# Optimization experiments

Hardware: AMD Instinct MI355X
Metric: run time of the kernel (lower is better)

Reference implementation:

```python
import jax, jax.numpy as jnp
import numpy as np

H = 1024     # hidden_size
NH = 16      # num heads
HD = H // NH # head_dim = 64
I = 4096     # intermediate_size
EPS = 1e-6


def rmsnorm(x, w, eps=EPS):
    var = jnp.mean(jnp.square(x), axis=-1, keepdims=True)
    return x * jax.lax.rsqrt(var + eps) * w


def attention(x, ctx, wq, wk, wv, wo):
    # x: [B,S,H], ctx: [B,Skv,H]; weights stored [in,out]
    B, S, _ = x.shape
    Skv = ctx.shape[1]
    q = (x @ wq).reshape(B, S, NH, HD)
    k = (ctx @ wk).reshape(B, Skv, NH, HD)
    v = (ctx @ wv).reshape(B, Skv, NH, HD)
    scores = jnp.einsum('bqhd,bkhd->bhqk', q, k) * (HD ** -0.5)
    attn = jax.nn.softmax(scores.astype(jnp.float32), axis=-1).astype(q.dtype)
    out = jnp.einsum('bhqk,bkhd->bqhd', attn, v).reshape(B, S, NH * HD)
    return out @ wo


def mlp(x, wg, wu, wd):
    return (jax.nn.silu(x @ wg) * (x @ wu)) @ wd


def setup_inputs() -> dict:
    key = jax.random.key(0)
    ks = jax.random.split(key, 16)
    p = lambda k, shape: (jax.random.normal(k, shape, jnp.float32) * 0.02)
    return {
        'hidden_states': jax.random.normal(ks[0], (1, 2048, H), jnp.float32),
        'context': jax.random.normal(ks[1], (1, 2048, H), jnp.float32),
        'sa_norm_w': jnp.ones((H,), jnp.float32),
        'sa_wq': p(ks[2], (H, NH * HD)),
        'sa_wk': p(ks[3], (H, NH * HD)),
        'sa_wv': p(ks[4], (H, NH * HD)),
        'sa_wo': p(ks[5], (NH * HD, H)),
        'ca_norm_w': jnp.ones((H,), jnp.float32),
        'ca_wq': p(ks[6], (H, NH * HD)),
        'ca_wk': p(ks[7], (H, NH * HD)),
        'ca_wv': p(ks[8], (H, NH * HD)),
        'ca_wo': p(ks[9], (NH * HD, H)),
        'mlp_norm_w': jnp.ones((H,), jnp.float32),
        'w_gate': p(ks[10], (H, I)),
        'w_up': p(ks[11], (H, I)),
        'w_down': p(ks[12], (I, H)),
    }


def reference(hidden_states, context, sa_norm_w, sa_wq, sa_wk, sa_wv, sa_wo,
              ca_norm_w, ca_wq, ca_wk, ca_wv, ca_wo,
              mlp_norm_w, w_gate, w_up, w_down):
    # self-attention block
    residual = hidden_states
    h = rmsnorm(hidden_states, sa_norm_w)
    h = residual + attention(h, h, sa_wq, sa_wk, sa_wv, sa_wo)
    # cross-attention block
    residual = h
    hn = rmsnorm(h, ca_norm_w)
    h = residual + attention(hn, context, ca_wq, ca_wk, ca_wv, ca_wo)
    # MLP block
    residual = h
    hn = rmsnorm(h, mlp_norm_w)
    h = residual + mlp(hn, w_gate, w_up, w_down)
    return h
```

## Files before the change

kernel.cpp:

```cpp
#include <hip/hip_runtime.h>

#define H 1024
#define S 2048
#define NH 16
#define HD 64
#define ISZ 4096

typedef __attribute__((ext_vector_type(8))) short s8v;
typedef __attribute__((ext_vector_type(4))) short s4v;
typedef __attribute__((ext_vector_type(4))) float f4v;

__device__ __forceinline__ short f2bf(float f) {
    unsigned u = __builtin_bit_cast(unsigned, f);
    unsigned r = (u + 0x7FFFu + ((u >> 16) & 1u)) >> 16;
    return (short)r;
}
__device__ __forceinline__ float bf2f(short s) {
    unsigned u = ((unsigned)(unsigned short)s) << 16;
    return __builtin_bit_cast(float, u);
}

__device__ __forceinline__ void gload_lds16(const short* g, short* l) {
    __builtin_amdgcn_global_load_lds(
        (const __attribute__((address_space(1))) void*)g,
        (__attribute__((address_space(3))) void*)l, 16, 0, 0);
}

struct PreArgs {
    const void* hid; const void* ctx;
    const void* sanw; const void* canw; const void* mlpnw;
    const void* w[11];
    short* hidc; short* ctxc; short* xn;
    short* canw_o; short* mlpnw_o;
    short* wT[11];
    int* flag_out;
};

__device__ __forceinline__ void tr_tile(const void* src, short* dst, int K, int N,
                                        int k0, int n0, int rmul, int roff,
                                        int isbf, float* tile ) {
    int t = threadIdx.x;
    int c = t & 31, r0 = t >> 5;
    if (isbf) {
        const short* s = (const short*)src;
#pragma unroll
        for (int i = 0; i < 4; i++)
            tile[(r0 + i * 8) * 33 + c] = bf2f(s[(k0 + r0 + i * 8) * N + n0 + c]);
    } else {
        const float* s = (const float*)src;
#pragma unroll
        for (int i = 0; i < 4; i++)
            tile[(r0 + i * 8) * 33 + c] = s[(k0 + r0 + i * 8) * N + n0 + c];
    }
    __syncthreads();
#pragma unroll
    for (int i = 0; i < 4; i++)
        dst[((n0 + r0 + i * 8) * rmul + roff) * K + k0 + c] = f2bf(tile[c * 33 + r0 + i * 8]);
}

__global__ __launch_bounds__(256) void preamble_kernel(PreArgs pa) {
    __shared__ float tile[32 * 33];
    __shared__ float red[4];
    int b = blockIdx.x;
    int t = threadIdx.x;
    int isbf = (((const unsigned*)pa.sanw)[0] == 0x3F803F80u);
    if (blockIdx.x == 0 && t == 0) pa.flag_out[0] = isbf;

    if (b < 2048) {
        int row = b;
        float xf[4];
        if (isbf) {
            s4v xv = *(const s4v*)((const short*)pa.hid + row * H + t * 4);
#pragma unroll
            for (int j = 0; j < 4; j++) xf[j] = bf2f(xv[j]);
        } else {
            const float* s = (const float*)pa.hid + row * H + t * 4;
#pragma unroll
            for (int j = 0; j < 4; j++) xf[j] = s[j];
        }
        float ss = 0.f;
        s4v cv;
#pragma unroll
        for (int j = 0; j < 4; j++) { cv[j] = f2bf(xf[j]); xf[j] = bf2f(cv[j]); ss += xf[j] * xf[j]; }
        *(s4v*)(pa.hidc + row * H + t * 4) = cv;
        int lane = t & 63, wid = t >> 6;
#pragma unroll
        for (int off = 32; off >= 1; off >>= 1) ss += __shfl_xor(ss, off);
        if (lane == 0) red[wid] = ss;
        __syncthreads();
        float tot = red[0] + red[1] + red[2] + red[3];
        float scale = rsqrtf(tot * (1.f / (float)H) + 1e-6f);
        float wv[4];
        if (isbf) {
            s4v wq = *(const s4v*)((const short*)pa.sanw + t * 4);
#pragma unroll
            for (int j = 0; j < 4; j++) wv[j] = bf2f(wq[j]);
        } else {
            const float* s = (const float*)pa.sanw + t * 4;
#pragma unroll
            for (int j = 0; j < 4; j++) wv[j] = s[j];
        }
        s4v ov;
#pragma unroll
        for (int j = 0; j < 4; j++) ov[j] = f2bf(xf[j] * scale * wv[j]);
        *(s4v*)(pa.xn + row * H + t * 4) = ov;
        return;
    }
    b -= 2048;
    if (b < 1024) {
        int i8 = b * 2048 + t * 8;
        if (isbf) {
            *(s8v*)(pa.ctxc + i8) = *(const s8v*)((const short*)pa.ctx + i8);
        } else {
            const float* s = (const float*)pa.ctx;
            s8v o;
#pragma unroll
            for (int j = 0; j < 8; j++) o[j] = f2bf(s[i8 + j]);
            *(s8v*)(pa.ctxc + i8) = o;
        }
        return;
    }
    b -= 1024;
    if (b < 2) {
        const void* src = (b == 0) ? pa.canw : pa.mlpnw;
        short* dst = (b == 0) ? pa.canw_o : pa.mlpnw_o;
        if (isbf) { if (t * 4 < H) *(s4v*)(dst + t * 4) = *(const s4v*)((const short*)src + t * 4); }
        else {
            const float* s = (const float*)src;
            s4v o;
#pragma unroll
            for (int j = 0; j < 4; j++) o[j] = f2bf(s[t * 4 + j]);
            *(s4v*)(dst + t * 4) = o;
        }
        return;
    }
    b -= 2;
    if (b < 8 * 1024) {
        int w = b >> 10, tl = b & 1023;
        tr_tile(pa.w[w], pa.wT[w], H, H, (tl & 31) * 32, (tl >> 5) * 32, 1, 0, isbf, tile);
        return;
    }
    b -= 8 * 1024;
    if (b < 2 * 4096) {
        int w = 8 + (b >> 12), tl = b & 4095;
        tr_tile(pa.w[w], pa.wT[8], H, ISZ, (tl & 31) * 32, (tl >> 5) * 32, 2, w - 8, isbf, tile);
        return;
    }
    b -= 2 * 4096;
    {
        tr_tile(pa.w[10], pa.wT[10], ISZ, H, (b & 127) * 32, (b >> 7) * 32, 1, 0, isbf, tile);
    }
}

__global__ __launch_bounds__(256) void rmsnorm_kernel(const short* __restrict__ x,
                                                      const short* __restrict__ w,
                                                      short* __restrict__ out) {
    int row = blockIdx.x;
    int t = threadIdx.x;
    int lane = t & 63, wid = t >> 6;
    const short* xr = x + row * H;

    s4v xv = *(const s4v*)(xr + t * 4);
    float xf[4];
    float ss = 0.f;
#pragma unroll
    for (int j = 0; j < 4; j++) { xf[j] = bf2f(xv[j]); ss += xf[j] * xf[j]; }
#pragma unroll
    for (int off = 32; off >= 1; off >>= 1) ss += __shfl_xor(ss, off);

    __shared__ float red[4];
    if (lane == 0) red[wid] = ss;
    __syncthreads();
    float tot = red[0] + red[1] + red[2] + red[3];
    float scale = rsqrtf(tot * (1.f / (float)H) + 1e-6f);

    s4v wv = *(const s4v*)(w + t * 4);
    s4v ov;
#pragma unroll
    for (int j = 0; j < 4; j++) ov[j] = f2bf(xf[j] * scale * bf2f(wv[j]));
    *(s4v*)(out + row * H + t * 4) = ov;
}

template <int BM_, int BN_>
__global__ __launch_bounds__(512, 2) void gemm_bt_kernel(
    const short* __restrict__ A0, const short* __restrict__ A1, int split, int lda,
    const short* __restrict__ Bt,
    void* __restrict__ C, int ldc, int K,
    const short* __restrict__ res,
    const int* __restrict__ dtype_flag,
    short* __restrict__ vtbuf, int vcol0,
    short* __restrict__ silu_out) {

    constexpr int MC = BM_ / 32;
    constexpr int NC = BN_ / 64;
    constexpr int U  = (BM_ + BN_) / 8;
    constexpr int PT = U / 8;
    constexpr int BUF = (BM_ + BN_) * 64;

    __shared__ short lds[2 * BUF];

    const short* A = (blockIdx.y < split) ? A0 : A1;
    int m0 = blockIdx.x * BM_;
    int n0 = blockIdx.y * BN_;

    int t = threadIdx.x;
    int lane = t & 63, wid = t >> 6;
    int quad = lane >> 4, l15 = lane & 15;
    int wr = wid >> 2, wc = wid & 3;
    int ld4 = lane >> 2, lc8 = (lane & 3) * 8;

    f4v acc[MC][NC] = {};

    auto stage = [&](short* buf, int k0) {
#pragma unroll
        for (int s = 0; s < PT; ++s) {
            int u = wid * PT + s;
            if (u < BM_ / 8) {
                int h = u / (BM_ / 16), r16 = u % (BM_ / 16);
                gload_lds16(A + (m0 + r16 * 16 + ld4) * lda + k0 + h * 32 + lc8,
                            buf + h * (BM_ * 32) + r16 * 512);
            } else {
                int ub = u - BM_ / 8;
                int h = ub / (BN_ / 16), r16 = ub % (BN_ / 16);
                gload_lds16(Bt + (n0 + r16 * 16 + ld4) * K + k0 + h * 32 + lc8,
                            buf + BM_ * 64 + h * (BN_ * 32) + r16 * 512);
            }
        }
    };

    auto compute = [&](const short* buf) {
#pragma unroll
        for (int kh = 0; kh < 2; ++kh) {
            s8v af[MC], bfv[NC];
#pragma unroll
            for (int mc = 0; mc < MC; ++mc)
                af[mc] = *(const s8v*)(buf + kh * (BM_ * 32) +
                                       (wr * (BM_ / 2) + mc * 16 + l15) * 32 + quad * 8);
#pragma unroll
            for (int nc = 0; nc < NC; ++nc)
                bfv[nc] = *(const s8v*)(buf + BM_ * 64 + kh * (BN_ * 32) +
                                        (wc * (BN_ / 4) + nc * 16 + l15) * 32 + quad * 8);
#pragma unroll
            for (int mc = 0; mc < MC; ++mc)
#pragma unroll
                for (int nc = 0; nc < NC; ++nc)
                    acc[mc][nc] = __builtin_amdgcn_mfma_f32_16x16x32_bf16(af[mc], bfv[nc], acc[mc][nc], 0, 0, 0);
        }
    };

    const int KT = K / 64;
    stage(lds, 0);
    __syncthreads();
    int cur = 0;
    for (int kt = 0; kt < KT - 1; ++kt) {
        stage(lds + (cur ^ 1) * BUF, (kt + 1) * 64);
        compute(lds + cur * BUF);
        __syncthreads();
        cur ^= 1;
    }
    compute(lds + cur * BUF);

    if (silu_out) {
#pragma unroll
        for (int mc = 0; mc < MC; mc++) {
#pragma unroll
            for (int nc = 0; nc < NC; nc++) {
                int row = m0 + wr * (BM_ / 2) + mc * 16 + quad * 4;
                int col = n0 + wc * (BN_ / 4) + nc * 16 + l15;
#pragma unroll
                for (int r = 0; r < 4; r++) {
                    float v = acc[mc][nc][r];
                    float other = __shfl_xor(v, 1);
                    if ((l15 & 1) == 0) {
                        float sig = 1.f / (1.f + __expf(-v));
                        silu_out[(row + r) * ISZ + (col >> 1)] = f2bf(v * sig * other);
                    }
                }
            }
        }
        return;
    }

    int out_fp32 = (dtype_flag != nullptr) && (dtype_flag[0] == 0);

#pragma unroll
    for (int mc = 0; mc < MC; mc++) {
#pragma unroll
        for (int nc = 0; nc < NC; nc++) {
            int row = m0 + wr * (BM_ / 2) + mc * 16 + quad * 4;
            int col = n0 + wc * (BN_ / 4) + nc * 16 + l15;
#pragma unroll
            for (int r = 0; r < 4; r++) {
                float vf = acc[mc][nc][r];
                if (res) vf += bf2f(res[(row + r) * ldc + col]);
                if (vtbuf && col >= vcol0)
                    vtbuf[(col - vcol0) * S + row + r] = f2bf(vf);
                else if (out_fp32)
                    ((float*)C)[(row + r) * ldc + col] = vf;
                else
                    ((short*)C)[(row + r) * ldc + col] = f2bf(vf);
            }
        }
    }
}

__global__ __launch_bounds__(256) void flash_attn_kernel(const short* __restrict__ q,
                                                         const short* __restrict__ k,
                                                         const short* __restrict__ vt,
                                                         int rs,
                                                         short* __restrict__ o) {
    int h = blockIdx.y;
    int q0 = blockIdx.x * 64;
    int t = threadIdx.x;
    int lane = t & 63, wid = t >> 6;
    int quad = lane >> 4, l15 = lane & 15;

    __shared__ short K2[2 * 128 * 32];
    __shared__ short V2[4 * 64 * 32];
    __shared__ short Pw[4][2048];

    int ld4 = lane >> 2, lc8 = (lane & 3) * 8;

    s8v bq[2];
    int qrow = q0 + wid * 16 + l15;
#pragma unroll
    for (int c = 0; c < 2; c++) {
        s8v raw = *(const s8v*)(q + qrow * rs + h * HD + c * 32 + quad * 8);
#pragma unroll
        for (int j = 0; j < 8; j++) bq[c][j] = f2bf(0.125f * bf2f(raw[j]));
    }

    f4v o_acc[4] = {};
    float m_s = -INFINITY, l_s = 0.f;

    for (int kv0 = 0; kv0 < S; kv0 += 128) {
#pragma unroll
        for (int dc = 0; dc < 2; dc++)
#pragma unroll
            for (int i = 0; i < 2; i++)
                gload_lds16(k + (kv0 + wid * 32 + i * 16 + ld4) * rs + h * HD + dc * 32 + lc8,
                            K2 + dc * 4096 + (wid * 32 + i * 16) * 32);
#pragma unroll
        for (int kc2 = 0; kc2 < 4; kc2++)
            gload_lds16(vt + (h * HD + wid * 16 + ld4) * S + kv0 + kc2 * 32 + lc8,
                        V2 + kc2 * 2048 + (wid * 16) * 32);
        __syncthreads();

        f4v st[8];
#pragma unroll
        for (int kc = 0; kc < 8; kc++) {
            f4v a_ = (f4v){0.f, 0.f, 0.f, 0.f};
#pragma unroll
            for (int dc = 0; dc < 2; dc++) {
                s8v kf = *(const s8v*)(K2 + dc * 4096 + (kc * 16 + l15) * 32 + quad * 8);
                a_ = __builtin_amdgcn_mfma_f32_16x16x32_bf16(kf, bq[dc], a_, 0, 0, 0);
            }
            st[kc] = a_;
        }

        float mloc = -INFINITY;
#pragma unroll
        for (int kc = 0; kc < 8; kc++)
#pragma unroll
            for (int r = 0; r < 4; r++) mloc = fmaxf(mloc, st[kc][r]);
        mloc = fmaxf(mloc, __shfl_xor(mloc, 16));
        mloc = fmaxf(mloc, __shfl_xor(mloc, 32));
        float m_new = fmaxf(m_s, mloc);
        float alpha = __expf(m_s - m_new);
        float lloc = 0.f;
#pragma unroll
        for (int kc = 0; kc < 8; kc++)
#pragma unroll
            for (int r = 0; r < 4; r++) {
                float p = __expf(st[kc][r] - m_new);
                st[kc][r] = p;
                lloc += p;
            }
        lloc += __shfl_xor(lloc, 16);
        lloc += __shfl_xor(lloc, 32);
        l_s = l_s * alpha + lloc;
        m_s = m_new;
#pragma unroll
        for (int nd = 0; nd < 4; nd++)
#pragma unroll
            for (int r = 0; r < 4; r++) o_acc[nd][r] *= alpha;

#pragma unroll
        for (int kc = 0; kc < 8; kc++)
#pragma unroll
            for (int r = 0; r < 4; r++)
                Pw[wid][(kc >> 1) * 512 + l15 * 32 + (kc & 1) * 16 + quad * 4 + r] = f2bf(st[kc][r]);

#pragma unroll
        for (int nd = 0; nd < 4; nd++) {
#pragma unroll
            for (int kc2 = 0; kc2 < 4; kc2++) {
                s8v vf = *(const s8v*)(V2 + kc2 * 2048 + (nd * 16 + l15) * 32 + quad * 8);
                s8v pf = *(const s8v*)(Pw[wid] + kc2 * 512 + l15 * 32 + quad * 8);
                o_acc[nd] = __builtin_amdgcn_mfma_f32_16x16x32_bf16(vf, pf, o_acc[nd], 0, 0, 0);
            }
        }
        __syncthreads();
    }

    float inv = 1.f / l_s;
#pragma unroll
    for (int nd = 0; nd < 4; nd++)
#pragma unroll
        for (int r = 0; r < 4; r++)
            Pw[wid][l15 * 64 + nd * 16 + quad * 4 + r] = f2bf(o_acc[nd][r] * inv);

    int qr = lane >> 2, dc2 = (lane & 3) * 16;
    s8v x0 = *(const s8v*)(Pw[wid] + qr * 64 + dc2);
    s8v x1 = *(const s8v*)(Pw[wid] + qr * 64 + dc2 + 8);
    short* dst = o + (q0 + wid * 16 + qr) * H + h * HD + dc2;
    *(s8v*)(dst) = x0;
    *(s8v*)(dst + 8) = x1;
}

extern "C" void kernel_launch(void* const* d_in, const int* in_sizes, int n_in,
                              void* d_out, int out_size, void* d_ws, size_t ws_size,
                              hipStream_t stream) {
    const int SH = S * H;
    const int WH = H * H;
    const int WI = H * ISZ;

    int* flag = (int*)d_ws;
    short* base = (short*)d_ws + 16;

    short* hidc   = base;
    short* ctxc   = hidc + SH;
    short* sanw   = ctxc + SH;
    short* canw   = sanw + H;
    short* mlpnw  = canw + H;
    short* saqkvT = mlpnw + H;
    short* sawoT  = saqkvT + 3 * WH;
    short* caqkvT = sawoT + WH;
    short* cawoT  = caqkvT + 3 * WH;
    short* wguT   = cawoT + WH;
    short* wdT    = wguT + 2 * WI;
    short* xn     = wdT + WI;
    short* qkv    = xn + SH;
    short* ao     = qkv + 3 * SH;
    short* h1     = ao + SH;
    short* gu     = qkv;
    short* h2     = qkv + 8 * SH;
    short* vt     = h2 + SH;

    dim3 blk(256);
    dim3 blk2(512);

    PreArgs pa;
    pa.hid = d_in[0]; pa.ctx = d_in[1];
    pa.sanw = d_in[2]; pa.canw = d_in[7]; pa.mlpnw = d_in[12];
    const void* wsrc[11] = {d_in[3], d_in[4], d_in[5], d_in[6],
                            d_in[8], d_in[9], d_in[10], d_in[11],
                            d_in[13], d_in[14], d_in[15]};
    short* wdst[11] = {saqkvT, saqkvT + WH, saqkvT + 2 * WH, sawoT,
                       caqkvT, caqkvT + WH, caqkvT + 2 * WH, cawoT,
                       wguT, wguT , wdT};
    for (int i = 0; i < 11; i++) { pa.w[i] = wsrc[i]; pa.wT[i] = wdst[i]; }
    pa.hidc = hidc; pa.ctxc = ctxc; pa.xn = xn;
    pa.canw_o = canw; pa.mlpnw_o = mlpnw;
    pa.flag_out = flag;
    const int pre_blocks = 2048 + 1024 + 2 + 8 * 1024 + 2 * 4096 + 4096;
    preamble_kernel<<<pre_blocks, blk, 0, stream>>>(pa);

    gemm_bt_kernel<128, 128><<<dim3(S / 128, 3 * H / 128), blk2, 0, stream>>>(
        xn, xn, 24, H, saqkvT, qkv, 3 * H, H, nullptr, nullptr, vt, 2 * H, nullptr);
    flash_attn_kernel<<<dim3(S / 64, NH), blk, 0, stream>>>(qkv, qkv + H, vt, 3 * H, ao);
    gemm_bt_kernel<64, 128><<<dim3(S / 64, H / 128), blk2, 0, stream>>>(
        ao, ao, 8, H, sawoT, h1, H, H, hidc, nullptr, nullptr, 0, nullptr);

    rmsnorm_kernel<<<S, blk, 0, stream>>>(h1, canw, xn);
    gemm_bt_kernel<128, 128><<<dim3(S / 128, 3 * H / 128), blk2, 0, stream>>>(
        xn, ctxc, 8, H, caqkvT, qkv, 3 * H, H, nullptr, nullptr, vt, 2 * H, nullptr);
    flash_attn_kernel<<<dim3(S / 64, NH), blk, 0, stream>>>(qkv, qkv + H, vt, 3 * H, ao);
    gemm_bt_kernel<64, 128><<<dim3(S / 64, H / 128), blk2, 0, stream>>>(
        ao, ao, 8, H, cawoT, h2, H, H, h1, nullptr, nullptr, 0, nullptr);

    rmsnorm_kernel<<<S, blk, 0, stream>>>(h2, mlpnw, xn);
    gemm_bt_kernel<256, 256><<<dim3(S / 256, 2 * ISZ / 256), blk2, 0, stream>>>(
        xn, xn, 32, H, wguT, nullptr, 2 * ISZ, H, nullptr, nullptr, nullptr, 0, gu);
    gemm_bt_kernel<64, 128><<<dim3(S / 64, H / 128), blk2, 0, stream>>>(
        gu, gu, 8, ISZ, wdT, d_out, H, ISZ, h2, flag, nullptr, 0, nullptr);
}
```

Baseline: 484.7 us.

## Restructure flash attention with split-KV waves, double-buffered swizzled LDS, exp2

The flash attention kernel now runs 8 waves per block, with two groups each handling half of the KV sequence. Their partial softmax states are merged through LDS at the end. K/V tiles are double-buffered so the next tile's global-to-LDS load overlaps compute, and an XOR swizzle is meant to avoid LDS bank conflicts. The softmax uses hardware exp2 with log2e folded into the Q scale, and packed bf16 conversion writes P. It costs more LDS per block plus an extra merge step at the end.

```diff
diff --git a/kernel.cpp b/kernel.cpp
--- a/kernel.cpp
+++ b/kernel.cpp
@@ -9,6 +9,7 @@
 typedef __attribute__((ext_vector_type(8))) short s8v;
 typedef __attribute__((ext_vector_type(4))) short s4v;
 typedef __attribute__((ext_vector_type(4))) float f4v;
+typedef __attribute__((ext_vector_type(2))) unsigned u2v;
 
 __device__ __forceinline__ short f2bf(float f) {
     unsigned u = __builtin_bit_cast(unsigned, f);
@@ -18,6 +19,12 @@
 __device__ __forceinline__ float bf2f(short s) {
     unsigned u = ((unsigned)(unsigned short)s) << 16;
     return __builtin_bit_cast(float, u);
+}
+__device__ __forceinline__ float exp2_hw(float x) {
+    float r; asm("v_exp_f32 %0, %1" : "=v"(r) : "v"(x)); return r;
+}
+__device__ __forceinline__ unsigned cvt_pk_bf16(float lo, float hi) {
+    unsigned r; asm("v_cvt_pk_bf16_f32 %0, %1, %2" : "=v"(r) : "v"(lo), "v"(hi)); return r;
 }
 
 __device__ __forceinline__ void gload_lds16(const short* g, short* l) {
@@ -304,55 +311,67 @@
     }
 }
 
-__global__ __launch_bounds__(256) void flash_attn_kernel(const short* __restrict__ q,
-                                                         const short* __restrict__ k,
-                                                         const short* __restrict__ vt,
-                                                         int rs,
-                                                         short* __restrict__ o) {
+__global__ __launch_bounds__(512, 4) void flash_attn_kernel(const short* __restrict__ q,
+                                                            const short* __restrict__ kk,
+                                                            const short* __restrict__ vt,
+                                                            int rs,
+                                                            short* __restrict__ o) {
+    __shared__ short lds[40960];
+
     int h = blockIdx.y;
     int q0 = blockIdx.x * 64;
     int t = threadIdx.x;
     int lane = t & 63, wid = t >> 6;
     int quad = lane >> 4, l15 = lane & 15;
-
-    __shared__ short K2[2 * 128 * 32];
-    __shared__ short V2[4 * 64 * 32];
-    __shared__ short Pw[4][2048];
-
-    int ld4 = lane >> 2, lc8 = (lane & 3) * 8;
-
+    int gw = wid & 3, gh = wid >> 2;
+    int kvbase = gh * 1024;
+    int kro = l15 & 7;
+
+    int lrow = lane >> 3;
+    int lsrc = ((lane & 7) ^ lrow) * 8;
+
+    auto stageKV = [&](int buf, int tt) {
+        int kvt = kvbase + tt * 64;
+        short* kb = lds + (gh * 2 + buf) * 4096;
+        short* vb = lds + 16384 + (gh * 2 + buf) * 4096;
+#pragma unroll
+        for (int i = 0; i < 2; i++) {
+            int r0 = gw * 16 + i * 8;
+            gload_lds16(kk + (kvt + r0 + lrow) * rs + h * HD + lsrc, kb + r0 * 64);
+            gload_lds16(vt + (h * HD + r0 + lrow) * S + kvt + lsrc, vb + r0 * 64);
+        }
+    };
+
+    const float qscale = 0.125f * 1.44269504f;
     s8v bq[2];
-    int qrow = q0 + wid * 16 + l15;
+    int qrow = q0 + gw * 16 + l15;
 #pragma unroll
     for (int c = 0; c < 2; c++) {
         s8v raw = *(const s8v*)(q + qrow * rs + h * HD + c * 32 + quad * 8);
 #pragma unroll
-        for (int j = 0; j < 8; j++) bq[c][j] = f2bf(0.125f * bf2f(raw[j]));
+        for (int j = 0; j < 8; j++) bq[c][j] = f2bf(qscale * bf2f(raw[j]));
     }
 
     f4v o_acc[4] = {};
     float m_s = -INFINITY, l_s = 0.f;
-
-    for (int kv0 = 0; kv0 < S; kv0 += 128) {
-#pragma unroll
-        for (int dc = 0; dc < 2; dc++)
-#pragma unroll
-            for (int i = 0; i < 2; i++)
-                gload_lds16(k + (kv0 + wid * 32 + i * 16 + ld4) * rs + h * HD + dc * 32 + lc8,
-                            K2 + dc * 4096 + (wid * 32 + i * 16) * 32);
-#pragma unroll
-        for (int kc2 = 0; kc2 < 4; kc2++)
-            gload_lds16(vt + (h * HD + wid * 16 + ld4) * S + kv0 + kc2 * 32 + lc8,
-                        V2 + kc2 * 2048 + (wid * 16) * 32);
-        __syncthreads();
-
-        f4v st[8];
-#pragma unroll
-        for (int kc = 0; kc < 8; kc++) {
+    short* pw = lds + 32768 + wid * 1024;
+
+    const int NT = 16;
+    stageKV(0, 0);
+    __syncthreads();
+    int cur = 0;
+    for (int tt = 0; tt < NT; ++tt) {
+        if (tt + 1 < NT) stageKV(cur ^ 1, tt + 1);
+        const short* kb = lds + (gh * 2 + cur) * 4096;
+        const short* vb = lds + 16384 + (gh * 2 + cur) * 4096;
+
+        f4v st[4];
+#pragma unroll
+        for (int kc = 0; kc < 4; kc++) {
             f4v a_ = (f4v){0.f, 0.f, 0.f, 0.f};
 #pragma unroll
             for (int dc = 0; dc < 2; dc++) {
-                s8v kf = *(const s8v*)(K2 + dc * 4096 + (kc * 16 + l15) * 32 + quad * 8);
+                s8v kf = *(const s8v*)(kb + (kc * 16 + l15) * 64 + ((dc * 4 + quad) ^ kro) * 8);
                 a_ = __builtin_amdgcn_mfma_f32_16x16x32_bf16(kf, bq[dc], a_, 0, 0, 0);
             }
             st[kc] = a_;
@@ -360,19 +379,19 @@
 
         float mloc = -INFINITY;
 #pragma unroll
-        for (int kc = 0; kc < 8; kc++)
+        for (int kc = 0; kc < 4; kc++)
 #pragma unroll
             for (int r = 0; r < 4; r++) mloc = fmaxf(mloc, st[kc][r]);
         mloc = fmaxf(mloc, __shfl_xor(mloc, 16));
         mloc = fmaxf(mloc, __shfl_xor(mloc, 32));
         float m_new = fmaxf(m_s, mloc);
-        float alpha = __expf(m_s - m_new);
+        float alpha = exp2_hw(m_s - m_new);
         float lloc = 0.f;
 #pragma unroll
-        for (int kc = 0; kc < 8; kc++)
+        for (int kc = 0; kc < 4; kc++)
 #pragma unroll
             for (int r = 0; r < 4; r++) {
-                float p = __expf(st[kc][r] - m_new);
+                float p = exp2_hw(st[kc][r] - m_new);
                 st[kc][r] = p;
                 lloc += p;
             }
@@ -386,33 +405,60 @@
             for (int r = 0; r < 4; r++) o_acc[nd][r] *= alpha;
 
 #pragma unroll
-        for (int kc = 0; kc < 8; kc++)
-#pragma unroll
-            for (int r = 0; r < 4; r++)
-                Pw[wid][(kc >> 1) * 512 + l15 * 32 + (kc & 1) * 16 + quad * 4 + r] = f2bf(st[kc][r]);
+        for (int kc = 0; kc < 4; kc++) {
+            u2v w;
+            w[0] = cvt_pk_bf16(st[kc][0], st[kc][1]);
+            w[1] = cvt_pk_bf16(st[kc][2], st[kc][3]);
+            int pslot = (kc * 2 + (quad >> 1)) ^ kro;
+            *(u2v*)(pw + l15 * 64 + pslot * 8 + (quad & 1) * 4) = w;
+        }
 
 #pragma unroll
         for (int nd = 0; nd < 4; nd++) {
 #pragma unroll
-            for (int kc2 = 0; kc2 < 4; kc2++) {
-                s8v vf = *(const s8v*)(V2 + kc2 * 2048 + (nd * 16 + l15) * 32 + quad * 8);
-                s8v pf = *(const s8v*)(Pw[wid] + kc2 * 512 + l15 * 32 + quad * 8);
+            for (int kc2 = 0; kc2 < 2; kc2++) {
+                s8v vf = *(const s8v*)(vb + (nd * 16 + l15) * 64 + ((kc2 * 4 + quad) ^ kro) * 8);
+                s8v pf = *(const s8v*)(pw + l15 * 64 + ((kc2 * 4 + quad) ^ kro) * 8);
                 o_acc[nd] = __builtin_amdgcn_mfma_f32_16x16x32_bf16(vf, pf, o_acc[nd], 0, 0, 0);
             }
         }
         __syncthreads();
-    }
-
-    float inv = 1.f / l_s;
+        cur ^= 1;
+    }
+
+    float* ex = (float*)lds;
+    if (gh == 1) {
+        int base = (gw * 64 + lane) * 20;
+#pragma unroll
+        for (int nd = 0; nd < 4; nd++) *(f4v*)(ex + base + nd * 4) = o_acc[nd];
+        ex[base + 16] = m_s;
+        ex[base + 17] = l_s;
+    }
+    __syncthreads();
+    if (gh == 1) return;
+
+    int base = (wid * 64 + lane) * 20;
+    float mB = ex[base + 16], lB = ex[base + 17];
+    float M = fmaxf(m_s, mB);
+    float a = exp2_hw(m_s - M), bsc = exp2_hw(mB - M);
+    float inv = 1.f / (a * l_s + bsc * lB);
+#pragma unroll
+    for (int nd = 0; nd < 4; nd++) {
+        f4v ob = *(const f4v*)(ex + base + nd * 4);
+#pragma unroll
+        for (int r = 0; r < 4; r++)
+            o_acc[nd][r] = (a * o_acc[nd][r] + bsc * ob[r]) * inv;
+    }
+
 #pragma unroll
     for (int nd = 0; nd < 4; nd++)
 #pragma unroll
         for (int r = 0; r < 4; r++)
-            Pw[wid][l15 * 64 + nd * 16 + quad * 4 + r] = f2bf(o_acc[nd][r] * inv);
+            pw[l15 * 64 + nd * 16 + quad * 4 + r] = f2bf(o_acc[nd][r]);
 
     int qr = lane >> 2, dc2 = (lane & 3) * 16;
-    s8v x0 = *(const s8v*)(Pw[wid] + qr * 64 + dc2);
-    s8v x1 = *(const s8v*)(Pw[wid] + qr * 64 + dc2 + 8);
+    s8v x0 = *(const s8v*)(pw + qr * 64 + dc2);
+    s8v x1 = *(const s8v*)(pw + qr * 64 + dc2 + 8);
     short* dst = o + (q0 + wid * 16 + qr) * H + h * HD + dc2;
     *(s8v*)(dst) = x0;
     *(s8v*)(dst + 8) = x1;
@@ -468,14 +514,14 @@
 
     gemm_bt_kernel<128, 128><<<dim3(S / 128, 3 * H / 128), blk2, 0, stream>>>(
         xn, xn, 24, H, saqkvT, qkv, 3 * H, H, nullptr, nullptr, vt, 2 * H, nullptr);
-    flash_attn_kernel<<<dim3(S / 64, NH), blk, 0, stream>>>(qkv, qkv + H, vt, 3 * H, ao);
+    flash_attn_kernel<<<dim3(S / 64, NH), blk2, 0, stream>>>(qkv, qkv + H, vt, 3 * H, ao);
     gemm_bt_kernel<64, 128><<<dim3(S / 64, H / 128), blk2, 0, stream>>>(
         ao, ao, 8, H, sawoT, h1, H, H, hidc, nullptr, nullptr, 0, nullptr);
 
     rmsnorm_kernel<<<S, blk, 0, stream>>>(h1, canw, xn);
     gemm_bt_kernel<128, 128><<<dim3(S / 128, 3 * H / 128), blk2, 0, stream>>>(
         xn, ctxc, 8, H, caqkvT, qkv, 3 * H, H, nullptr, nullptr, vt, 2 * H, nullptr);
-    flash_attn_kernel<<<dim3(S / 64, NH), blk, 0, stream>>>(qkv, qkv + H, vt, 3 * H, ao);
+    flash_attn_kernel<<<dim3(S / 64, NH), blk2, 0, stream>>>(qkv, qkv + H, vt, 3 * H, ao);
     gemm_bt_kernel<64, 128><<<dim3(S / 64, H / 128), blk2, 0, stream>>>(
         ao, ao, 8, H, cawoT, h2, H, H, h1, nullptr, nullptr, 0, nullptr);
 
```

Result: faster. 458.6 us (-5.4%).
